# Kernel optimization log

Measured on AMD Instinct MI355X. Metric: run time of the kernel, lower is better.

Reference implementation:

```python
import jax, jax.numpy as jnp
import numpy as np

BETA = 0.9          # snn.Leaky beta
THRESH = 1.0        # snnTorch default threshold
ALPHA = 2.0         # surrogate.atan default alpha
NUM_STEPS = 10
IN_DIM, H1, H2, NUM_CLASSES = 128, 64, 32, 4
BATCH = 131072


def heaviside(x):
    return (x > THRESH).astype(x.dtype)


def lif_step(cur, mem):
    # snnTorch Leaky (reset_mechanism='subtract'): reset computed from
    # previous membrane (detached), then mem = beta*mem + cur - reset*thr,
    # spike fired from the new membrane.
    reset = heaviside(mem)
    mem_new = BETA * mem + cur - reset * THRESH
    spk = heaviside(mem_new)
    return spk, mem_new


def setup_inputs() -> dict:
    key = jax.random.key(0)
    ks = jax.random.split(key, 7)
    s1 = 1.0 / np.sqrt(IN_DIM)
    s2 = 1.0 / np.sqrt(H1)
    s3 = 1.0 / np.sqrt(H2)
    return {
        "x": jax.random.normal(ks[0], (BATCH, IN_DIM), dtype=jnp.float32),
        "w1": jax.random.uniform(ks[1], (H1, IN_DIM), jnp.float32, -s1, s1),
        "b1": jax.random.uniform(ks[2], (H1,), jnp.float32, -s1, s1),
        "w2": jax.random.uniform(ks[3], (H2, H1), jnp.float32, -s2, s2),
        "b2": jax.random.uniform(ks[4], (H2,), jnp.float32, -s2, s2),
        "w3": jax.random.uniform(ks[5], (NUM_CLASSES, H2), jnp.float32, -s3, s3),
        "b3": jax.random.uniform(ks[6], (NUM_CLASSES,), jnp.float32, -s3, s3),
    }


def reference(x, w1, b1, w2, b2, w3, b3):
    B = x.shape[0]
    dt = x.dtype
    # fc1(x) is loop-invariant in the original forward; compute once.
    cur1 = x @ w1.T + b1  # [B, 64]

    def step(carry, _):
        mem1, mem2, mem3, spk_sum = carry
        spk1, mem1 = lif_step(cur1, mem1)
        cur2 = spk1 @ w2.T + b2          # [B, 32]
        spk2, mem2 = lif_step(cur2, mem2)
        cur3 = spk2 @ w3.T + b3          # [B, num_classes]
        mem3 = mem3 * 0.9 + cur3
        spk_sum = spk_sum + mem3
        return (mem1, mem2, mem3, spk_sum), None

    init = (
        jnp.zeros((B, w1.shape[0]), dt),
        jnp.zeros((B, w2.shape[0]), dt),
        jnp.zeros((B, w3.shape[0]), dt),
        jnp.zeros((B, w3.shape[0]), dt),
    )
    (_, _, _, spk_sum), _ = jax.lax.scan(step, init, None, length=NUM_STEPS)
    return spk_sum / NUM_STEPS
```

## Files before the change

### kernel.cpp

```cpp
#include <hip/hip_runtime.h>


#define NBLK 2048

typedef __attribute__((ext_vector_type(4))) int i32x4;

__device__ __forceinline__ unsigned prm(unsigned hi, unsigned lo, unsigned sel) {
    return __builtin_amdgcn_perm(hi, lo, sel);
}

__global__ void snn_prep(const float* __restrict__ w1, const float* __restrict__ b1,
                         const float* __restrict__ w2, unsigned char* __restrict__ wsb) {
    int tid = threadIdx.x;
    for (int it = tid; it < 8192; it += 256) {
        int n = it >> 7, k = it & 127;
        int V = (int)llround((double)w1[n * 128 + k] * 0x1p34);
        int nt = n >> 4, m = n & 15, kt = k >> 6, kgp = (k >> 4) & 3, e = k & 15;
        unsigned base = (unsigned)(((nt * 2 + kt) * 4) << 10) + (unsigned)(((kgp << 4) | m) * 16 + e);
#pragma unroll
        for (int p = 0; p < 4; ++p) {
            int d = ((V + 128) & 255) - 128; V = (V - d) >> 8;
            wsb[base + ((unsigned)p << 10)] = (unsigned char)d;
        }
    }
    for (int it = tid; it < 2048; it += 256) {
        int n = it >> 6, k = it & 63;
        int V = (int)llround((double)w2[n * 64 + k] * 0x1p33);
        int nt2 = n >> 4, c = n & 15, kgp = k >> 4, e = k & 15;
        unsigned base = 32768u + (unsigned)((nt2 * 4) << 10) + (unsigned)(((kgp << 4) | c) * 16 + e);
#pragma unroll
        for (int p = 0; p < 4; ++p) {
            int d = ((V + 128) & 255) - 128; V = (V - d) >> 8;
            wsb[base + ((unsigned)p << 10)] = (unsigned char)d;
        }
    }
    if (tid < 64) {
        long long s = 0;
        for (int k = 0; k < 128; ++k) s += llround((double)w1[tid * 128 + k] * 0x1p34);
        double* biasd = (double*)(wsb + 40960);
        biasd[tid] = (double)b1[tid] + 1082163328.0 * (double)s * 0x1p-61;
    }
}

__global__ __launch_bounds__(256, 1) void snn_main(
    const float* __restrict__ x,
    const float* __restrict__ b2,
    const float* __restrict__ w3,
    const float* __restrict__ b3,
    const unsigned char* __restrict__ wsb,
    float* __restrict__ out)
{
    __shared__ __align__(16) unsigned char sS[4][10240];

    const int tid  = threadIdx.x;
    const int wave = tid >> 6;
    const int lane = tid & 63;
    const int m15  = lane & 15;
    const int kg   = lane >> 4;
    const int swz  = (m15 >> 1) & 3;
    unsigned char* sw = sS[wave];
    const int r0 = blockIdx.x * 64 + wave * 16;

    i32x4 bx[2][4];
#pragma unroll
    for (int kt = 0; kt < 2; ++kt) {
        const float4* xp = (const float4*)(x + (size_t)(r0 + m15) * 128 + kt * 64 + kg * 16);
        float4 q0 = xp[0], q1 = xp[1], q2 = xp[2], q3 = xp[3];
        unsigned o0[4], o1[4], o2[4], o3[4];
#pragma unroll
        for (int g = 0; g < 4; ++g) {
            float f0 = (g == 0 ? q0.x : g == 1 ? q1.x : g == 2 ? q2.x : q3.x);
            float f1 = (g == 0 ? q0.y : g == 1 ? q1.y : g == 2 ? q2.y : q3.y);
            float f2 = (g == 0 ? q0.z : g == 1 ? q1.z : g == 2 ? q2.z : q3.z);
            float f3 = (g == 0 ? q0.w : g == 1 ? q1.w : g == 2 ? q2.w : q3.w);
            unsigned V0 = ((unsigned)(__float2int_rn(f0 * 0x1p27f) + 0x40000000)) ^ 0x80808080u;
            unsigned V1 = ((unsigned)(__float2int_rn(f1 * 0x1p27f) + 0x40000000)) ^ 0x80808080u;
            unsigned V2 = ((unsigned)(__float2int_rn(f2 * 0x1p27f) + 0x40000000)) ^ 0x80808080u;
            unsigned V3 = ((unsigned)(__float2int_rn(f3 * 0x1p27f) + 0x40000000)) ^ 0x80808080u;
            unsigned A01 = prm(V1, V0, 0x05010400u), A23 = prm(V3, V2, 0x05010400u);
            unsigned B01 = prm(V1, V0, 0x07030602u), B23 = prm(V3, V2, 0x07030602u);
            o0[g] = prm(A23, A01, 0x05040100u);
            o1[g] = prm(A23, A01, 0x07060302u);
            o2[g] = prm(B23, B01, 0x05040100u);
            o3[g] = prm(B23, B01, 0x07060302u);
        }
        bx[kt][0] = (i32x4){(int)o0[0], (int)o0[1], (int)o0[2], (int)o0[3]};
        bx[kt][1] = (i32x4){(int)o1[0], (int)o1[1], (int)o1[2], (int)o1[3]};
        bx[kt][2] = (i32x4){(int)o2[0], (int)o2[1], (int)o2[2], (int)o2[3]};
        bx[kt][3] = (i32x4){(int)o3[0], (int)o3[1], (int)o3[2], (int)o3[3]};
    }

    const double* biasd = (const double*)(wsb + 40960);

#pragma unroll
    for (int nt1 = 0; nt1 < 4; ++nt1) {
        i32x4 aw[2][4];
#pragma unroll
        for (int kt = 0; kt < 2; ++kt)
#pragma unroll
            for (int p = 0; p < 4; ++p)
                aw[kt][p] = *(const i32x4*)(wsb + (unsigned)(((nt1 * 2 + kt) * 4 + p) << 10) + lane * 16);

        i32x4 acc0 = {0,0,0,0}, acc1 = {0,0,0,0}, acc2 = {0,0,0,0}, acc3 = {0,0,0,0}, acc4 = {0,0,0,0};
#pragma unroll
        for (int kt = 0; kt < 2; ++kt) {
            acc0 = __builtin_amdgcn_mfma_i32_16x16x64_i8(aw[kt][0], bx[kt][2], acc0, 0, 0, 0);
            acc0 = __builtin_amdgcn_mfma_i32_16x16x64_i8(aw[kt][1], bx[kt][1], acc0, 0, 0, 0);
            acc0 = __builtin_amdgcn_mfma_i32_16x16x64_i8(aw[kt][2], bx[kt][0], acc0, 0, 0, 0);
            acc1 = __builtin_amdgcn_mfma_i32_16x16x64_i8(aw[kt][0], bx[kt][3], acc1, 0, 0, 0);
            acc1 = __builtin_amdgcn_mfma_i32_16x16x64_i8(aw[kt][1], bx[kt][2], acc1, 0, 0, 0);
            acc1 = __builtin_amdgcn_mfma_i32_16x16x64_i8(aw[kt][2], bx[kt][1], acc1, 0, 0, 0);
            acc1 = __builtin_amdgcn_mfma_i32_16x16x64_i8(aw[kt][3], bx[kt][0], acc1, 0, 0, 0);
            acc2 = __builtin_amdgcn_mfma_i32_16x16x64_i8(aw[kt][1], bx[kt][3], acc2, 0, 0, 0);
            acc2 = __builtin_amdgcn_mfma_i32_16x16x64_i8(aw[kt][2], bx[kt][2], acc2, 0, 0, 0);
            acc2 = __builtin_amdgcn_mfma_i32_16x16x64_i8(aw[kt][3], bx[kt][1], acc2, 0, 0, 0);
            acc3 = __builtin_amdgcn_mfma_i32_16x16x64_i8(aw[kt][2], bx[kt][3], acc3, 0, 0, 0);
            acc3 = __builtin_amdgcn_mfma_i32_16x16x64_i8(aw[kt][3], bx[kt][2], acc3, 0, 0, 0);
            acc4 = __builtin_amdgcn_mfma_i32_16x16x64_i8(aw[kt][3], bx[kt][3], acc4, 0, 0, 0);
        }
        double c[4], mem[4];
        bool rst[4];
#pragma unroll
        for (int j = 0; j < 4; ++j) {
            c[j] = biasd[nt1 * 16 + kg * 4 + j]
                 + (double)acc0[j] * 0x1p-45 + (double)acc1[j] * 0x1p-37
                 + (double)acc2[j] * 0x1p-29 + (double)acc3[j] * 0x1p-21
                 + (double)acc4[j] * 0x1p-13;
            mem[j] = 0.0; rst[j] = false;
        }
        const int wbase = ((nt1 ^ swz) << 4) + kg * 4;
#pragma unroll
        for (int t = 0; t < 10; ++t) {
            unsigned sb = 0u;
#pragma unroll
            for (int j = 0; j < 4; ++j) {
                double t2 = __fma_rn(0.9, mem[j], c[j]);
                mem[j] = rst[j] ? (t2 - 1.0) : t2;
                rst[j] = mem[j] > 1.0;
                sb |= rst[j] ? (1u << (8 * j)) : 0u;
            }
            *(unsigned*)(sw + (t * 16 + m15) * 64 + wbase) = sb;
        }
    }

    asm volatile("s_waitcnt lgkmcnt(0)" ::: "memory");
    __builtin_amdgcn_sched_barrier(0);

    i32x4 w2f[2][4];
#pragma unroll
    for (int nt2 = 0; nt2 < 2; ++nt2)
#pragma unroll
        for (int p = 0; p < 4; ++p)
            w2f[nt2][p] = *(const i32x4*)(wsb + 32768u + (unsigned)((nt2 * 4 + p) << 10) + lane * 16);

    const double b2d0 = (double)b2[m15];
    const double b2d1 = (double)b2[m15 + 16];
    float w3lo[4], w3hi[4], b3c[4];
#pragma unroll
    for (int cc = 0; cc < 4; ++cc) {
        w3lo[cc] = w3[cc * 32 + m15];
        w3hi[cc] = w3[cc * 32 + m15 + 16];
        b3c[cc]  = (float)((double)b3[cc] * 41.381059609);
    }

    const float CTf[10] = {6.5132156f, 6.1257951f, 5.6953279f, 5.2170310f, 4.6855900f,
                           4.0951000f, 3.4390000f, 2.7100000f, 1.9000000f, 1.0000000f};
    double mem2[8] = {0,0,0,0,0,0,0,0};
    float  z[8]    = {0,0,0,0,0,0,0,0};
    bool   rs2[8]  = {false,false,false,false,false,false,false,false};

#pragma unroll
    for (int t = 0; t < 10; ++t) {
        i32x4 a = *(const i32x4*)(sw + (t * 16 + m15) * 64 + ((kg ^ swz) << 4));
#pragma unroll
        for (int nt2 = 0; nt2 < 2; ++nt2) {
            i32x4 p0 = {0,0,0,0}, p1 = {0,0,0,0}, p2 = {0,0,0,0}, p3 = {0,0,0,0};
            p0 = __builtin_amdgcn_mfma_i32_16x16x64_i8(a, w2f[nt2][0], p0, 0, 0, 0);
            p1 = __builtin_amdgcn_mfma_i32_16x16x64_i8(a, w2f[nt2][1], p1, 0, 0, 0);
            p2 = __builtin_amdgcn_mfma_i32_16x16x64_i8(a, w2f[nt2][2], p2, 0, 0, 0);
            p3 = __builtin_amdgcn_mfma_i32_16x16x64_i8(a, w2f[nt2][3], p3, 0, 0, 0);
            const double b2d = nt2 ? b2d1 : b2d0;
#pragma unroll
            for (int j = 0; j < 4; ++j) {
                const int s = nt2 * 4 + j;
                int lo = p0[j] + p1[j] * 256 + p2[j] * 65536;
                double cv = __fma_rn((double)lo, 0x1p-33,
                            __fma_rn((double)p3[j], 0x1p-9, b2d));
                double t2 = __fma_rn(0.9, mem2[s], cv);
                mem2[s] = rs2[s] ? (t2 - 1.0) : t2;
                rs2[s] = mem2[s] > 1.0;
                z[s] += rs2[s] ? CTf[t] : 0.0f;
            }
        }
    }

#pragma unroll
    for (int j = 0; j < 4; ++j) {
        float red[4];
#pragma unroll
        for (int cc = 0; cc < 4; ++cc) {
            float v = z[j] * w3lo[cc] + z[4 + j] * w3hi[cc];
            v += __shfl_xor(v, 1);
            v += __shfl_xor(v, 2);
            v += __shfl_xor(v, 4);
            v += __shfl_xor(v, 8);
            red[cc] = (v + b3c[cc]) * 0.1f;
        }
        if (m15 == 0) {
            float4 o4 = {red[0], red[1], red[2], red[3]};
            *(float4*)(out + (size_t)(r0 + kg * 4 + j) * 4) = o4;
        }
    }
}

extern "C" void kernel_launch(void* const* d_in, const int* in_sizes, int n_in,
                              void* d_out, int out_size, void* d_ws, size_t ws_size,
                              hipStream_t stream) {
    const float* x  = (const float*)d_in[0];
    const float* w1 = (const float*)d_in[1];
    const float* b1 = (const float*)d_in[2];
    const float* w2 = (const float*)d_in[3];
    const float* b2 = (const float*)d_in[4];
    const float* w3 = (const float*)d_in[5];
    const float* b3 = (const float*)d_in[6];
    unsigned char* wsb = (unsigned char*)d_ws;
    float* out = (float*)d_out;

    snn_prep<<<1, 256, 0, stream>>>(w1, b1, w2, wsb);
    snn_main<<<NBLK, 256, 0, stream>>>(x, b2, w3, b3, wsb, out);
}
```

Measured before the change: 109.7 us.

## Use single-wave blocks and reorder layer-2 loops to cut register pressure

Switches from 256-thread blocks (four waves, each with its own LDS slice) to 64-thread single-wave blocks, so four times as many blocks are launched. Each block needs a quarter of the shared memory, and launch bounds of 64 may let more waves reside per CU. The layer-2 loop now runs over the two output tiles first, loading only that tile's w2 fragments and keeping four membrane states instead of eight, with sched barriers added to limit live ranges. The trade-off is reloading each spike tile from LDS twice and paying more per-block launch overhead.

Result: no change. 107.9 us (-1.7%).

```diff
diff --git a/kernel.cpp b/kernel.cpp
--- a/kernel.cpp
+++ b/kernel.cpp
@@ -1,7 +1,7 @@
 #include <hip/hip_runtime.h>
 
 
-#define NBLK 2048
+#define NBLK 8192
 
 typedef __attribute__((ext_vector_type(4))) int i32x4;
 
@@ -42,7 +42,7 @@
     }
 }
 
-__global__ __launch_bounds__(256, 1) void snn_main(
+__global__ __launch_bounds__(64, 1) void snn_main(
     const float* __restrict__ x,
     const float* __restrict__ b2,
     const float* __restrict__ w3,
@@ -50,16 +50,13 @@
     const unsigned char* __restrict__ wsb,
     float* __restrict__ out)
 {
-    __shared__ __align__(16) unsigned char sS[4][10240];
-
-    const int tid  = threadIdx.x;
-    const int wave = tid >> 6;
-    const int lane = tid & 63;
+    __shared__ __align__(16) unsigned char sS[10240];
+
+    const int lane = threadIdx.x;
     const int m15  = lane & 15;
     const int kg   = lane >> 4;
     const int swz  = (m15 >> 1) & 3;
-    unsigned char* sw = sS[wave];
-    const int r0 = blockIdx.x * 64 + wave * 16;
+    const int r0 = blockIdx.x * 16;
 
     i32x4 bx[2][4];
 #pragma unroll
@@ -139,19 +136,13 @@
                 rst[j] = mem[j] > 1.0;
                 sb |= rst[j] ? (1u << (8 * j)) : 0u;
             }
-            *(unsigned*)(sw + (t * 16 + m15) * 64 + wbase) = sb;
-        }
+            *(unsigned*)(sS + (t * 16 + m15) * 64 + wbase) = sb;
+        }
+        __builtin_amdgcn_sched_barrier(0);
     }
 
     asm volatile("s_waitcnt lgkmcnt(0)" ::: "memory");
     __builtin_amdgcn_sched_barrier(0);
-
-    i32x4 w2f[2][4];
-#pragma unroll
-    for (int nt2 = 0; nt2 < 2; ++nt2)
-#pragma unroll
-        for (int p = 0; p < 4; ++p)
-            w2f[nt2][p] = *(const i32x4*)(wsb + 32768u + (unsigned)((nt2 * 4 + p) << 10) + lane * 16);
 
     const double b2d0 = (double)b2[m15];
     const double b2d1 = (double)b2[m15 + 16];
@@ -163,35 +154,41 @@
         b3c[cc]  = (float)((double)b3[cc] * 41.381059609);
     }
 
-    const float CTf[10] = {6.5132156f, 6.1257951f, 5.6953279f, 5.2170310f, 4.6855900f,
-                           4.0951000f, 3.4390000f, 2.7100000f, 1.9000000f, 1.0000000f};
-    double mem2[8] = {0,0,0,0,0,0,0,0};
-    float  z[8]    = {0,0,0,0,0,0,0,0};
-    bool   rs2[8]  = {false,false,false,false,false,false,false,false};
-
-#pragma unroll
-    for (int t = 0; t < 10; ++t) {
-        i32x4 a = *(const i32x4*)(sw + (t * 16 + m15) * 64 + ((kg ^ swz) << 4));
-#pragma unroll
-        for (int nt2 = 0; nt2 < 2; ++nt2) {
+    float z[8] = {0,0,0,0,0,0,0,0};
+#pragma unroll
+    for (int nt2 = 0; nt2 < 2; ++nt2) {
+        i32x4 w2f[4];
+#pragma unroll
+        for (int p = 0; p < 4; ++p)
+            w2f[p] = *(const i32x4*)(wsb + 32768u + (unsigned)((nt2 * 4 + p) << 10) + lane * 16);
+        const double b2d = nt2 ? b2d1 : b2d0;
+        double mem2[4] = {0,0,0,0};
+        bool rs2[4] = {false,false,false,false};
+#pragma unroll
+        for (int t = 0; t < 10; ++t) {
+            i32x4 a = *(const i32x4*)(sS + (t * 16 + m15) * 64 + ((kg ^ swz) << 4));
             i32x4 p0 = {0,0,0,0}, p1 = {0,0,0,0}, p2 = {0,0,0,0}, p3 = {0,0,0,0};
-            p0 = __builtin_amdgcn_mfma_i32_16x16x64_i8(a, w2f[nt2][0], p0, 0, 0, 0);
-            p1 = __builtin_amdgcn_mfma_i32_16x16x64_i8(a, w2f[nt2][1], p1, 0, 0, 0);
-            p2 = __builtin_amdgcn_mfma_i32_16x16x64_i8(a, w2f[nt2][2], p2, 0, 0, 0);
-            p3 = __builtin_amdgcn_mfma_i32_16x16x64_i8(a, w2f[nt2][3], p3, 0, 0, 0);
-            const double b2d = nt2 ? b2d1 : b2d0;
+            p0 = __builtin_amdgcn_mfma_i32_16x16x64_i8(a, w2f[0], p0, 0, 0, 0);
+            p1 = __builtin_amdgcn_mfma_i32_16x16x64_i8(a, w2f[1], p1, 0, 0, 0);
+            p2 = __builtin_amdgcn_mfma_i32_16x16x64_i8(a, w2f[2], p2, 0, 0, 0);
+            p3 = __builtin_amdgcn_mfma_i32_16x16x64_i8(a, w2f[3], p3, 0, 0, 0);
+            const float CTt = (t == 0) ? 6.5132156f : (t == 1) ? 6.1257951f :
+                              (t == 2) ? 5.6953279f : (t == 3) ? 5.2170310f :
+                              (t == 4) ? 4.6855900f : (t == 5) ? 4.0951000f :
+                              (t == 6) ? 3.4390000f : (t == 7) ? 2.7100000f :
+                              (t == 8) ? 1.9000000f : 1.0f;
 #pragma unroll
             for (int j = 0; j < 4; ++j) {
-                const int s = nt2 * 4 + j;
                 int lo = p0[j] + p1[j] * 256 + p2[j] * 65536;
                 double cv = __fma_rn((double)lo, 0x1p-33,
                             __fma_rn((double)p3[j], 0x1p-9, b2d));
-                double t2 = __fma_rn(0.9, mem2[s], cv);
-                mem2[s] = rs2[s] ? (t2 - 1.0) : t2;
-                rs2[s] = mem2[s] > 1.0;
-                z[s] += rs2[s] ? CTf[t] : 0.0f;
+                double t2 = __fma_rn(0.9, mem2[j], cv);
+                mem2[j] = rs2[j] ? (t2 - 1.0) : t2;
+                rs2[j] = mem2[j] > 1.0;
+                z[nt2 * 4 + j] += rs2[j] ? CTt : 0.0f;
             }
         }
+        __builtin_amdgcn_sched_barrier(0);
     }
 
 #pragma unroll
@@ -227,5 +224,5 @@
     float* out = (float*)d_out;
 
     snn_prep<<<1, 256, 0, stream>>>(w1, b1, w2, wsb);
-    snn_main<<<NBLK, 256, 0, stream>>>(x, b2, w3, b3, wsb, out);
-}
+    snn_main<<<NBLK, 64, 0, stream>>>(x, b2, w3, b3, wsb, out);
+}
```
